# Kernel tuning notes

Measured on AMD Instinct MI355X. Metric: run time of the kernel, lower is better.

Reference implementation:

```python
import math
import jax, jax.numpy as jnp
import numpy as np

D_MODEL = 1024
N_HEADS = 16
D_K = D_MODEL // N_HEADS
LQ, LK, B = 2048, 2048, 2


def setup_inputs() -> dict:
    key = jax.random.key(0)
    ks = jax.random.split(key, 12)
    q = jax.random.normal(ks[0], (LQ, B, D_MODEL), dtype=jnp.float32)
    k = jax.random.normal(ks[1], (LK, B, D_MODEL), dtype=jnp.float32)
    v = jax.random.normal(ks[2], (LK, B, D_MODEL), dtype=jnp.float32)
    # causal mask: scores with mask==0 are filled with -1e9
    mask = jnp.tril(jnp.ones((LQ, LK), dtype=jnp.int32))
    s = 0.02
    w_q = jax.random.normal(ks[3], (D_MODEL, D_MODEL), jnp.float32) * s
    b_q = jnp.zeros((D_MODEL,), jnp.float32)
    w_k = jax.random.normal(ks[4], (D_MODEL, D_MODEL), jnp.float32) * s
    b_k = jnp.zeros((D_MODEL,), jnp.float32)
    w_v = jax.random.normal(ks[5], (D_MODEL, D_MODEL), jnp.float32) * s
    b_v = jnp.zeros((D_MODEL,), jnp.float32)
    w_o = jax.random.normal(ks[6], (D_MODEL, D_MODEL), jnp.float32) * s
    b_o = jnp.zeros((D_MODEL,), jnp.float32)
    return {"query": q, "key": k, "value": v, "mask": mask,
            "w_q": w_q, "b_q": b_q, "w_k": w_k, "b_k": b_k,
            "w_v": w_v, "b_v": b_v, "w_o": w_o, "b_o": b_o}


def reference(query, key, value, mask, w_q, b_q, w_k, b_k, w_v, b_v, w_o, b_o):
    # dropout layers are identity (eval mode)
    Lq, Bsz, D = query.shape
    Lk = key.shape[0]
    scale = math.sqrt(D_K)
    # seq-first linear projections, then [L,B,D] -> [B,H,L,dk]
    def proj(x, w, b, L):
        y = x @ w.T + b
        return y.reshape(L, Bsz, N_HEADS, D_K).transpose(1, 2, 0, 3)
    Q = proj(query, w_q, b_q, Lq)   # [B,H,Lq,dk]
    K = proj(key, w_k, b_k, Lk)     # [B,H,Lk,dk]
    V = proj(value, w_v, b_v, Lk)   # [B,H,Lk,dk]
    scores = jnp.einsum('bhqd,bhkd->bhqk', Q, K) / scale
    m = mask[None, None, :, :]  # 2D mask broadcast path of original
    scores = jnp.where(m == 0, jnp.float32(-1e9), scores)
    attn = jax.nn.softmax(scores, axis=-1)  # [B,H,Lq,Lk]
    out = jnp.einsum('bhqk,bhkd->bhqd', attn, V)  # [B,H,Lq,dk]
    # replicate torch: transpose(0,1) -> [H,B,Lq,dk], flat view to [Lq,B,D]
    out = jnp.transpose(out, (1, 0, 2, 3)).reshape(Lq, Bsz, D)
    output = out @ w_o.T + b_o
    return output, attn
```

## Files before the change

kernel.cpp:

```cpp
#include <hip/hip_runtime.h>
#include <cstdint>

#define DM    1024
#define NH    16
#define DKH   64
#define SEQ   2048
#define BSZ   2
#define MROWS 4096
#define QB    128

typedef __attribute__((ext_vector_type(8))) short bf16x8;
typedef __attribute__((ext_vector_type(4))) float f32x4;

__device__ __forceinline__ f32x4 mfma16(bf16x8 a, bf16x8 b, f32x4 c){
  return __builtin_amdgcn_mfma_f32_16x16x32_bf16(a, b, c, 0, 0, 0);
}

__device__ __forceinline__ ushort f2bf(float f){
  unsigned u = __float_as_uint(f);
  return (ushort)((u + 0x7FFFu + ((u >> 16) & 1u)) >> 16);
}

__device__ __forceinline__ void gload16(const ushort* g, ushort* l){
  __builtin_amdgcn_global_load_lds(
      (const __attribute__((address_space(1))) void*)g,
      (__attribute__((address_space(3))) void*)l, 16, 0, 0);
}

__global__ void cast_all(const float* __restrict__ q, const float* __restrict__ k,
                         const float* __restrict__ v, const float* __restrict__ wq,
                         const float* __restrict__ wk, const float* __restrict__ wv,
                         const float* __restrict__ wo,
                         ushort* __restrict__ qb, ushort* __restrict__ kb,
                         ushort* __restrict__ vb, ushort* __restrict__ wqb,
                         ushort* __restrict__ wkb, ushort* __restrict__ wvb,
                         ushort* __restrict__ wob)
{
  const int NB = (MROWS*DM)/4;
  const int NW = (DM*DM)/4;
  int stride = gridDim.x*blockDim.x;
  for (int i = blockIdx.x*blockDim.x + threadIdx.x; i < 3*NB; i += stride){
    int sel = i >> 20, j = i & (NB-1);
    const float4 x = ((const float4*)(sel==0?q:sel==1?k:v))[j];
    ushort4 o; o.x=f2bf(x.x); o.y=f2bf(x.y); o.z=f2bf(x.z); o.w=f2bf(x.w);
    ((ushort4*)(sel==0?qb:sel==1?kb:vb))[j] = o;
  }
  for (int i = blockIdx.x*blockDim.x + threadIdx.x; i < 4*NW; i += stride){
    int sel = i >> 18, j = i & (NW-1);
    const float4 x = ((const float4*)(sel==0?wq:sel==1?wk:sel==2?wv:wo))[j];
    ushort4 o; o.x=f2bf(x.x); o.y=f2bf(x.y); o.z=f2bf(x.z); o.w=f2bf(x.w);
    ((ushort4*)(sel==0?wqb:sel==1?wkb:sel==2?wvb:wob))[j] = o;
  }
}

template<int OUT_F32>
__device__ __forceinline__ void gemm_body(const ushort* __restrict__ A,
                                          const ushort* __restrict__ W,
                                          const float* __restrict__ bias,
                                          void* __restrict__ outp)
{
  __shared__ ushort As[128*32];
  __shared__ ushort Bs[128*32];
  const int tid = threadIdx.x, w = tid>>6, l = tid&63;
  const int wr = w>>1, wc = w&1, lr = l&15, lg = l>>4;
  const int bm = blockIdx.x, bn = blockIdx.y;
  const ushort* Ab = A + (size_t)bm*128*DM;
  const ushort* Wb = W + (size_t)bn*128*DM;
  f32x4 z4 = {0.f,0.f,0.f,0.f};
  f32x4 acc[4][4];
  #pragma unroll
  for (int i=0;i<4;i++){ acc[i][0]=z4; acc[i][1]=z4; acc[i][2]=z4; acc[i][3]=z4; }

  for (int k0 = 0; k0 < DM; k0 += 32){
    __syncthreads();
    #pragma unroll
    for (int i=0;i<2;i++){
      int idx = w*2+i;
      int row = idx*16 + (l>>2);
      int cg  = (l&3)*8;
      gload16(&Ab[(size_t)row*DM + k0 + cg], &As[idx*512]);
      gload16(&Wb[(size_t)row*DM + k0 + cg], &Bs[idx*512]);
    }
    __syncthreads();
    bf16x8 af[4], bw[4];
    #pragma unroll
    for (int t=0;t<4;t++) af[t] = *(const bf16x8*)&As[(wr*64 + t*16 + lr)*32 + lg*8];
    #pragma unroll
    for (int t=0;t<4;t++) bw[t] = *(const bf16x8*)&Bs[(wc*64 + t*16 + lr)*32 + lg*8];
    #pragma unroll
    for (int tm=0;tm<4;tm++)
      #pragma unroll
      for (int tn=0;tn<4;tn++)
        acc[tm][tn] = mfma16(af[tm], bw[tn], acc[tm][tn]);
  }
  #pragma unroll
  for (int tn=0;tn<4;tn++){
    int col = bn*128 + wc*64 + tn*16 + lr;
    float bv = bias[col];
    #pragma unroll
    for (int tm=0;tm<4;tm++){
      #pragma unroll
      for (int r=0;r<4;r++){
        int row = bm*128 + wr*64 + tm*16 + lg*4 + r;
        float val = acc[tm][tn][r] + bv;
        if (OUT_F32) ((float*)outp)[(size_t)row*DM + col] = val;
        else ((ushort*)outp)[(size_t)row*DM + col] = f2bf(val);
      }
    }
  }
}

__global__ __launch_bounds__(256) void gemm_qkv(
    const ushort* __restrict__ A0, const ushort* __restrict__ A1, const ushort* __restrict__ A2,
    const ushort* __restrict__ W0, const ushort* __restrict__ W1, const ushort* __restrict__ W2,
    const float* __restrict__ b0, const float* __restrict__ b1, const float* __restrict__ b2,
    ushort* __restrict__ O0, ushort* __restrict__ O1, ushort* __restrict__ O2)
{
  int z = blockIdx.z;
  const ushort* A = (z==0)?A0:((z==1)?A1:A2);
  const ushort* W = (z==0)?W0:((z==1)?W1:W2);
  const float*  b = (z==0)?b0:((z==1)?b1:b2);
  ushort*       O = (z==0)?O0:((z==1)?O1:O2);
  gemm_body<0>(A, W, b, O);
}

__global__ __launch_bounds__(256) void gemm_fin(const ushort* __restrict__ A,
                                                const ushort* __restrict__ W,
                                                const float* __restrict__ b,
                                                float* __restrict__ O)
{
  gemm_body<1>(A, W, b, O);
}

__global__ __launch_bounds__(256) void transpose_v(const ushort* __restrict__ Vp,
                                                   ushort* __restrict__ Vt)
{
  __shared__ ushort Ts[64*72];
  const int lt = blockIdx.x;
  const int h  = blockIdx.y;
  const int b  = blockIdx.z;
  const int tid = threadIdx.x;
  const int sr = tid>>3, sc = (tid&7)*8;
  uint4 v0 = *(const uint4*)&Vp[((size_t)(lt*64+sr)*BSZ + b)*DM + h*DKH + sc];
  uint4 v1 = *(const uint4*)&Vp[((size_t)(lt*64+sr+32)*BSZ + b)*DM + h*DKH + sc];
  const ushort* p0 = (const ushort*)&v0;
  const ushort* p1 = (const ushort*)&v1;
  #pragma unroll
  for (int j=0;j<8;j++){
    Ts[(sc+j)*72 + sr]    = p0[j];
    Ts[(sc+j)*72 + sr+32] = p1[j];
  }
  __syncthreads();
  const size_t ob = (size_t)((b*NH+h)*DKH);
  *(uint4*)&Vt[(ob + sr)*SEQ + lt*64 + sc]    = *(const uint4*)&Ts[sr*72 + sc];
  *(uint4*)&Vt[(ob + sr+32)*SEQ + lt*64 + sc] = *(const uint4*)&Ts[(sr+32)*72 + sc];
}

__global__ __launch_bounds__(512) void attn_fused(const ushort* __restrict__ Qp,
                                                  const ushort* __restrict__ Kp,
                                                  const ushort* __restrict__ Vt,
                                                  float* __restrict__ attn,
                                                  ushort* __restrict__ ctx)
{
  __shared__ ushort Ks[64*72];
  __shared__ ushort Vs[64*72];
  __shared__ ushort Ps[8][16*72];
  const int bid0 = blockIdx.x;
  const int bid  = (bid0 & 7)*64 + (bid0 >> 3);
  const int qb = 15 - (bid & 15);
  const int h  = (bid>>4)&15, b = bid>>8;
  const int tid = threadIdx.x, w = tid>>6, l = tid&63;
  const int lr = l&15, lg = l>>4;
  const int q0 = qb*QB;
  const int sr = tid>>3, sc = (tid&7)*8;
  const int ntiles = 2*qb + 2;
  ushort* Pw = &Ps[w][0];
  const size_t attnBase = (size_t)(b*NH+h)*SEQ*SEQ;
  const size_t vtBase   = (size_t)((b*NH+h)*DKH);
  const int qrow = q0 + w*16;
  const int wmax = qrow + 15;

  bf16x8 aq0 = *(const bf16x8*)&Qp[((size_t)(qrow+lr)*BSZ + b)*DM + h*DKH + lg*8];
  bf16x8 aq1 = *(const bf16x8*)&Qp[((size_t)(qrow+lr)*BSZ + b)*DM + h*DKH + 32 + lg*8];

  float rs[4] = {0.f,0.f,0.f,0.f};
  for (int kt = 0; kt < ntiles; kt++){
    __syncthreads();
    *(uint4*)&Ks[sr*72+sc] = *(const uint4*)&Kp[((size_t)(kt*64+sr)*BSZ + b)*DM + h*DKH + sc];
    __syncthreads();
    if (kt*64 <= wmax){
      #pragma unroll
      for (int nt=0; nt<4; nt++){
        f32x4 s4 = {0.f,0.f,0.f,0.f};
        bf16x8 bk0 = *(const bf16x8*)&Ks[(nt*16+lr)*72 + lg*8];
        bf16x8 bk1 = *(const bf16x8*)&Ks[(nt*16+lr)*72 + 32 + lg*8];
        s4 = mfma16(aq0, bk0, s4);
        s4 = mfma16(aq1, bk1, s4);
        int kc = kt*64 + nt*16 + lr;
        #pragma unroll
        for (int r=0;r<4;r++){
          int qr = qrow + lg*4 + r;
          float e = exp2f(s4[r]*0.18033688011112042f);
          rs[r] += (kc <= qr) ? e : 0.f;
        }
      }
    }
  }
  float rinv[4];
  #pragma unroll
  for (int r=0;r<4;r++){
    float vs = rs[r];
    vs += __shfl_xor(vs, 1, 16);
    vs += __shfl_xor(vs, 2, 16);
    vs += __shfl_xor(vs, 4, 16);
    vs += __shfl_xor(vs, 8, 16);
    rinv[r] = 1.0f / vs;
  }

  f32x4 z4 = {0.f,0.f,0.f,0.f};
  f32x4 oacc[4] = {z4,z4,z4,z4};
  for (int kt = 0; kt < ntiles; kt++){
    __syncthreads();
    *(uint4*)&Ks[sr*72+sc] = *(const uint4*)&Kp[((size_t)(kt*64+sr)*BSZ + b)*DM + h*DKH + sc];
    *(uint4*)&Vs[sr*72+sc] = *(const uint4*)&Vt[(vtBase + sr)*SEQ + kt*64 + sc];
    __syncthreads();
    if (kt*64 <= wmax){
      #pragma unroll
      for (int nt=0; nt<4; nt++){
        f32x4 s4 = {0.f,0.f,0.f,0.f};
        bf16x8 bk0 = *(const bf16x8*)&Ks[(nt*16+lr)*72 + lg*8];
        bf16x8 bk1 = *(const bf16x8*)&Ks[(nt*16+lr)*72 + 32 + lg*8];
        s4 = mfma16(aq0, bk0, s4);
        s4 = mfma16(aq1, bk1, s4);
        int kc = kt*64 + nt*16 + lr;
        #pragma unroll
        for (int r=0;r<4;r++){
          int qg = qrow + lg*4 + r;
          float p = (kc <= qg) ? exp2f(s4[r]*0.18033688011112042f)*rinv[r] : 0.f;
          Pw[(lg*4+r)*72 + nt*16 + lr] = f2bf(p);
        }
      }
      #pragma unroll
      for (int pass=0; pass<4; pass++){
        int row = pass*4 + lg;
        ushort4 pv = *(const ushort4*)&Pw[row*72 + lr*4];
        float4 o;
        o.x = __uint_as_float(((unsigned)pv.x) << 16);
        o.y = __uint_as_float(((unsigned)pv.y) << 16);
        o.z = __uint_as_float(((unsigned)pv.z) << 16);
        o.w = __uint_as_float(((unsigned)pv.w) << 16);
        *(float4*)&attn[attnBase + (size_t)(qrow + row)*SEQ + kt*64 + lr*4] = o;
      }
      #pragma unroll
      for (int nt=0; nt<4; nt++){
        #pragma unroll
        for (int ss=0; ss<2; ss++){
          bf16x8 pa = *(const bf16x8*)&Pw[lr*72 + ss*32 + lg*8];
          bf16x8 vb = *(const bf16x8*)&Vs[(nt*16+lr)*72 + ss*32 + lg*8];
          oacc[nt] = mfma16(pa, vb, oacc[nt]);
        }
      }
    } else {
      float4 zz = {0.f,0.f,0.f,0.f};
      #pragma unroll
      for (int pass=0; pass<4; pass++){
        int row = pass*4 + lg;
        *(float4*)&attn[attnBase + (size_t)(qrow + row)*SEQ + kt*64 + lr*4] = zz;
      }
    }
  }
  #pragma unroll
  for (int nt=0;nt<4;nt++){
    #pragma unroll
    for (int r=0;r<4;r++){
      int qg = qrow + lg*4 + r;
      ctx[((size_t)(h*BSZ+b)*SEQ + qg)*DKH + nt*16 + lr] = f2bf(oacc[nt][r]);
    }
  }
  int z0 = ntiles*64;
  if (z0 < SEQ){
    float4 zz = {0.f,0.f,0.f,0.f};
    for (int r16=0; r16<16; r16++){
      float* rowp = attn + attnBase + (size_t)(qrow + r16)*SEQ;
      for (int c = z0 + l*4; c < SEQ; c += 256)
        *(float4*)&rowp[c] = zz;
    }
  }
}

extern "C" void kernel_launch(void* const* d_in, const int* in_sizes, int n_in,
                              void* d_out, int out_size, void* d_ws, size_t ws_size,
                              hipStream_t stream)
{
  (void)in_sizes; (void)n_in; (void)out_size; (void)ws_size;
  const float* q  = (const float*)d_in[0];
  const float* k  = (const float*)d_in[1];
  const float* v  = (const float*)d_in[2];
  const float* wq = (const float*)d_in[4];
  const float* bq = (const float*)d_in[5];
  const float* wk = (const float*)d_in[6];
  const float* bk = (const float*)d_in[7];
  const float* wv = (const float*)d_in[8];
  const float* bv = (const float*)d_in[9];
  const float* wo = (const float*)d_in[10];
  const float* bo = (const float*)d_in[11];

  char* ws = (char*)d_ws;
  const size_t SZ_BIG = (size_t)MROWS*DM*2;
  const size_t SZ_W   = (size_t)DM*DM*2;
  ushort* Qb  = (ushort*)(ws);
  ushort* Kb  = (ushort*)(ws + SZ_BIG);
  ushort* Vb  = (ushort*)(ws + 2*SZ_BIG);
  ushort* Wqb = (ushort*)(ws + 3*SZ_BIG);
  ushort* Wkb = (ushort*)(ws + 3*SZ_BIG + SZ_W);
  ushort* Wvb = (ushort*)(ws + 3*SZ_BIG + 2*SZ_W);
  ushort* Wob = (ushort*)(ws + 3*SZ_BIG + 3*SZ_W);
  ushort* Qp  = (ushort*)(ws + 3*SZ_BIG + 4*SZ_W);
  ushort* Kp  = (ushort*)(ws + 4*SZ_BIG + 4*SZ_W);
  ushort* Vp  = (ushort*)(ws + 5*SZ_BIG + 4*SZ_W);
  ushort* Ctx = (ushort*)(ws + 6*SZ_BIG + 4*SZ_W);
  ushort* Vt  = Qb;

  float* out  = (float*)d_out;
  float* attn = out + (size_t)SEQ*BSZ*DM;

  cast_all<<<2048, 256, 0, stream>>>(q,k,v,wq,wk,wv,wo, Qb,Kb,Vb,Wqb,Wkb,Wvb,Wob);
  dim3 gq(32, 8, 3);
  gemm_qkv<<<gq, 256, 0, stream>>>(Qb,Kb,Vb, Wqb,Wkb,Wvb, bq,bk,bv, Qp,Kp,Vp);
  dim3 gt(32, NH, BSZ);
  transpose_v<<<gt, 256, 0, stream>>>(Vp, Vt);
  attn_fused<<<512, 512, 0, stream>>>(Qp, Kp, Vt, attn, Ctx);
  dim3 gf(32, 8, 1);
  gemm_fin<<<gf, 256, 0, stream>>>(Ctx, Wob, bo, out);
}
```

Measured before the change: 261.1 us.

## Double K/V tile to 128 keys with register prefetch and nontemporal attn stores

Each loop round of the attention kernel now stages 128 keys instead of 64, which halves the number of barrier pairs. The next round's K and V tiles are prefetched into registers while the current round computes. The large attn probability writes switch to nontemporal stores to reduce cache pollution. Block-to-work mapping is changed so the query blocks of one (batch, head) land on the same XCD, and launch bounds now request 4 blocks per CU. The larger LDS footprint and extra prefetch registers may limit occupancy.

```diff
diff --git a/kernel.cpp b/kernel.cpp
--- a/kernel.cpp
+++ b/kernel.cpp
@@ -8,6 +8,7 @@
 #define BSZ   2
 #define MROWS 4096
 #define QB    128
+#define K2    128
 
 typedef __attribute__((ext_vector_type(8))) short bf16x8;
 typedef __attribute__((ext_vector_type(4))) float f32x4;
@@ -25,6 +26,10 @@
   __builtin_amdgcn_global_load_lds(
       (const __attribute__((address_space(1))) void*)g,
       (__attribute__((address_space(3))) void*)l, 16, 0, 0);
+}
+
+__device__ __forceinline__ void ntstore4(float* p, f32x4 v){
+  __builtin_nontemporal_store(v, (f32x4*)p);
 }
 
 __global__ void cast_all(const float* __restrict__ q, const float* __restrict__ k,
@@ -156,134 +161,165 @@
   *(uint4*)&Vt[(ob + sr+32)*SEQ + lt*64 + sc] = *(const uint4*)&Ts[(sr+32)*72 + sc];
 }
 
-__global__ __launch_bounds__(512) void attn_fused(const ushort* __restrict__ Qp,
-                                                  const ushort* __restrict__ Kp,
-                                                  const ushort* __restrict__ Vt,
-                                                  float* __restrict__ attn,
-                                                  ushort* __restrict__ ctx)
-{
-  __shared__ ushort Ks[64*72];
-  __shared__ ushort Vs[64*72];
+__global__ __launch_bounds__(512, 4) void attn_fused(const ushort* __restrict__ Qp,
+                                                     const ushort* __restrict__ Kp,
+                                                     const ushort* __restrict__ Vt,
+                                                     float* __restrict__ attn,
+                                                     ushort* __restrict__ ctx)
+{
+  __shared__ ushort Ks[K2*72];
+  __shared__ ushort Vs[64*136];
   __shared__ ushort Ps[8][16*72];
   const int bid0 = blockIdx.x;
-  const int bid  = (bid0 & 7)*64 + (bid0 >> 3);
-  const int qb = 15 - (bid & 15);
-  const int h  = (bid>>4)&15, b = bid>>8;
+  const int xcd = bid0 & 7, slot = bid0 >> 3;
+  const int grp = xcd + 8*(slot>>4);
+  const int qb  = 15 - (slot & 15);
+  const int h = grp & 15, b = grp >> 4;
   const int tid = threadIdx.x, w = tid>>6, l = tid&63;
   const int lr = l&15, lg = l>>4;
   const int q0 = qb*QB;
-  const int sr = tid>>3, sc = (tid&7)*8;
-  const int ntiles = 2*qb + 2;
+  const int rounds = qb + 1;
   ushort* Pw = &Ps[w][0];
   const size_t attnBase = (size_t)(b*NH+h)*SEQ*SEQ;
   const size_t vtBase   = (size_t)((b*NH+h)*DKH);
   const int qrow = q0 + w*16;
   const int wmax = qrow + 15;
 
+  const int sKr = tid>>3,  sKc = (tid&7)*8;
+  const int sVr = tid>>4,  sVc = (tid&15)*8;
+  const ushort* Kg = Kp + (size_t)b*DM + h*DKH;
+  const ushort* Vg = Vt + vtBase*SEQ;
+
   bf16x8 aq0 = *(const bf16x8*)&Qp[((size_t)(qrow+lr)*BSZ + b)*DM + h*DKH + lg*8];
   bf16x8 aq1 = *(const bf16x8*)&Qp[((size_t)(qrow+lr)*BSZ + b)*DM + h*DKH + 32 + lg*8];
 
   float rs[4] = {0.f,0.f,0.f,0.f};
-  for (int kt = 0; kt < ntiles; kt++){
-    __syncthreads();
-    *(uint4*)&Ks[sr*72+sc] = *(const uint4*)&Kp[((size_t)(kt*64+sr)*BSZ + b)*DM + h*DKH + sc];
-    __syncthreads();
-    if (kt*64 <= wmax){
+  uint4 ka0 = *(const uint4*)&Kg[(size_t)(sKr)*BSZ*DM + sKc];
+  uint4 ka1 = *(const uint4*)&Kg[(size_t)(sKr+64)*BSZ*DM + sKc];
+  for (int r = 0; r < rounds; r++){
+    __syncthreads();
+    *(uint4*)&Ks[sKr*72+sKc]      = ka0;
+    *(uint4*)&Ks[(sKr+64)*72+sKc] = ka1;
+    if (r+1 < rounds){
+      ka0 = *(const uint4*)&Kg[(size_t)((r+1)*K2+sKr)*BSZ*DM + sKc];
+      ka1 = *(const uint4*)&Kg[(size_t)((r+1)*K2+sKr+64)*BSZ*DM + sKc];
+    }
+    __syncthreads();
+    #pragma unroll
+    for (int hh=0; hh<2; hh++){
+      int kbase = r*K2 + hh*64;
+      if (kbase > wmax) break;
       #pragma unroll
       for (int nt=0; nt<4; nt++){
         f32x4 s4 = {0.f,0.f,0.f,0.f};
-        bf16x8 bk0 = *(const bf16x8*)&Ks[(nt*16+lr)*72 + lg*8];
-        bf16x8 bk1 = *(const bf16x8*)&Ks[(nt*16+lr)*72 + 32 + lg*8];
+        bf16x8 bk0 = *(const bf16x8*)&Ks[(hh*64+nt*16+lr)*72 + lg*8];
+        bf16x8 bk1 = *(const bf16x8*)&Ks[(hh*64+nt*16+lr)*72 + 32 + lg*8];
         s4 = mfma16(aq0, bk0, s4);
         s4 = mfma16(aq1, bk1, s4);
-        int kc = kt*64 + nt*16 + lr;
-        #pragma unroll
-        for (int r=0;r<4;r++){
-          int qr = qrow + lg*4 + r;
-          float e = exp2f(s4[r]*0.18033688011112042f);
-          rs[r] += (kc <= qr) ? e : 0.f;
+        int kc = kbase + nt*16 + lr;
+        #pragma unroll
+        for (int r4=0;r4<4;r4++){
+          int qr = qrow + lg*4 + r4;
+          float e = exp2f(s4[r4]*0.18033688011112042f);
+          rs[r4] += (kc <= qr) ? e : 0.f;
         }
       }
     }
   }
   float rinv[4];
   #pragma unroll
-  for (int r=0;r<4;r++){
-    float vs = rs[r];
+  for (int r4=0;r4<4;r4++){
+    float vs = rs[r4];
     vs += __shfl_xor(vs, 1, 16);
     vs += __shfl_xor(vs, 2, 16);
     vs += __shfl_xor(vs, 4, 16);
     vs += __shfl_xor(vs, 8, 16);
-    rinv[r] = 1.0f / vs;
+    rinv[r4] = 1.0f / vs;
   }
 
   f32x4 z4 = {0.f,0.f,0.f,0.f};
   f32x4 oacc[4] = {z4,z4,z4,z4};
-  for (int kt = 0; kt < ntiles; kt++){
-    __syncthreads();
-    *(uint4*)&Ks[sr*72+sc] = *(const uint4*)&Kp[((size_t)(kt*64+sr)*BSZ + b)*DM + h*DKH + sc];
-    *(uint4*)&Vs[sr*72+sc] = *(const uint4*)&Vt[(vtBase + sr)*SEQ + kt*64 + sc];
-    __syncthreads();
-    if (kt*64 <= wmax){
-      #pragma unroll
-      for (int nt=0; nt<4; nt++){
-        f32x4 s4 = {0.f,0.f,0.f,0.f};
-        bf16x8 bk0 = *(const bf16x8*)&Ks[(nt*16+lr)*72 + lg*8];
-        bf16x8 bk1 = *(const bf16x8*)&Ks[(nt*16+lr)*72 + 32 + lg*8];
-        s4 = mfma16(aq0, bk0, s4);
-        s4 = mfma16(aq1, bk1, s4);
-        int kc = kt*64 + nt*16 + lr;
-        #pragma unroll
-        for (int r=0;r<4;r++){
-          int qg = qrow + lg*4 + r;
-          float p = (kc <= qg) ? exp2f(s4[r]*0.18033688011112042f)*rinv[r] : 0.f;
-          Pw[(lg*4+r)*72 + nt*16 + lr] = f2bf(p);
+  uint4 kb0 = *(const uint4*)&Kg[(size_t)(sKr)*BSZ*DM + sKc];
+  uint4 kb1 = *(const uint4*)&Kg[(size_t)(sKr+64)*BSZ*DM + sKc];
+  uint4 vb0 = *(const uint4*)&Vg[(size_t)(sVr)*SEQ + sVc];
+  uint4 vb1 = *(const uint4*)&Vg[(size_t)(sVr+32)*SEQ + sVc];
+  for (int r = 0; r < rounds; r++){
+    __syncthreads();
+    *(uint4*)&Ks[sKr*72+sKc]        = kb0;
+    *(uint4*)&Ks[(sKr+64)*72+sKc]   = kb1;
+    *(uint4*)&Vs[sVr*136+sVc]       = vb0;
+    *(uint4*)&Vs[(sVr+32)*136+sVc]  = vb1;
+    if (r+1 < rounds){
+      kb0 = *(const uint4*)&Kg[(size_t)((r+1)*K2+sKr)*BSZ*DM + sKc];
+      kb1 = *(const uint4*)&Kg[(size_t)((r+1)*K2+sKr+64)*BSZ*DM + sKc];
+      vb0 = *(const uint4*)&Vg[(size_t)(sVr)*SEQ + (r+1)*K2 + sVc];
+      vb1 = *(const uint4*)&Vg[(size_t)(sVr+32)*SEQ + (r+1)*K2 + sVc];
+    }
+    __syncthreads();
+    #pragma unroll
+    for (int hh=0; hh<2; hh++){
+      int kbase = r*K2 + hh*64;
+      if (kbase <= wmax){
+        #pragma unroll
+        for (int nt=0; nt<4; nt++){
+          f32x4 s4 = {0.f,0.f,0.f,0.f};
+          bf16x8 bk0 = *(const bf16x8*)&Ks[(hh*64+nt*16+lr)*72 + lg*8];
+          bf16x8 bk1 = *(const bf16x8*)&Ks[(hh*64+nt*16+lr)*72 + 32 + lg*8];
+          s4 = mfma16(aq0, bk0, s4);
+          s4 = mfma16(aq1, bk1, s4);
+          int kc = kbase + nt*16 + lr;
+          #pragma unroll
+          for (int r4=0;r4<4;r4++){
+            int qg = qrow + lg*4 + r4;
+            float p = (kc <= qg) ? exp2f(s4[r4]*0.18033688011112042f)*rinv[r4] : 0.f;
+            Pw[(lg*4+r4)*72 + nt*16 + lr] = f2bf(p);
+          }
+        }
+        #pragma unroll
+        for (int pass=0; pass<4; pass++){
+          int row = pass*4 + lg;
+          ushort4 pv = *(const ushort4*)&Pw[row*72 + lr*4];
+          f32x4 o;
+          o.x = __uint_as_float(((unsigned)pv.x) << 16);
+          o.y = __uint_as_float(((unsigned)pv.y) << 16);
+          o.z = __uint_as_float(((unsigned)pv.z) << 16);
+          o.w = __uint_as_float(((unsigned)pv.w) << 16);
+          ntstore4(&attn[attnBase + (size_t)(qrow + row)*SEQ + kbase + lr*4], o);
+        }
+        bf16x8 pa0 = *(const bf16x8*)&Pw[lr*72 + lg*8];
+        bf16x8 pa1 = *(const bf16x8*)&Pw[lr*72 + 32 + lg*8];
+        #pragma unroll
+        for (int nt=0; nt<4; nt++){
+          bf16x8 vv0 = *(const bf16x8*)&Vs[(nt*16+lr)*136 + hh*64 + lg*8];
+          bf16x8 vv1 = *(const bf16x8*)&Vs[(nt*16+lr)*136 + hh*64 + 32 + lg*8];
+          oacc[nt] = mfma16(pa0, vv0, oacc[nt]);
+          oacc[nt] = mfma16(pa1, vv1, oacc[nt]);
+        }
+      } else {
+        f32x4 zz = {0.f,0.f,0.f,0.f};
+        #pragma unroll
+        for (int pass=0; pass<4; pass++){
+          int row = pass*4 + lg;
+          ntstore4(&attn[attnBase + (size_t)(qrow + row)*SEQ + kbase + lr*4], zz);
         }
       }
-      #pragma unroll
-      for (int pass=0; pass<4; pass++){
-        int row = pass*4 + lg;
-        ushort4 pv = *(const ushort4*)&Pw[row*72 + lr*4];
-        float4 o;
-        o.x = __uint_as_float(((unsigned)pv.x) << 16);
-        o.y = __uint_as_float(((unsigned)pv.y) << 16);
-        o.z = __uint_as_float(((unsigned)pv.z) << 16);
-        o.w = __uint_as_float(((unsigned)pv.w) << 16);
-        *(float4*)&attn[attnBase + (size_t)(qrow + row)*SEQ + kt*64 + lr*4] = o;
-      }
-      #pragma unroll
-      for (int nt=0; nt<4; nt++){
-        #pragma unroll
-        for (int ss=0; ss<2; ss++){
-          bf16x8 pa = *(const bf16x8*)&Pw[lr*72 + ss*32 + lg*8];
-          bf16x8 vb = *(const bf16x8*)&Vs[(nt*16+lr)*72 + ss*32 + lg*8];
-          oacc[nt] = mfma16(pa, vb, oacc[nt]);
-        }
-      }
-    } else {
-      float4 zz = {0.f,0.f,0.f,0.f};
-      #pragma unroll
-      for (int pass=0; pass<4; pass++){
-        int row = pass*4 + lg;
-        *(float4*)&attn[attnBase + (size_t)(qrow + row)*SEQ + kt*64 + lr*4] = zz;
-      }
     }
   }
   #pragma unroll
   for (int nt=0;nt<4;nt++){
     #pragma unroll
-    for (int r=0;r<4;r++){
-      int qg = qrow + lg*4 + r;
-      ctx[((size_t)(h*BSZ+b)*SEQ + qg)*DKH + nt*16 + lr] = f2bf(oacc[nt][r]);
-    }
-  }
-  int z0 = ntiles*64;
+    for (int r4=0;r4<4;r4++){
+      int qg = qrow + lg*4 + r4;
+      ctx[((size_t)(h*BSZ+b)*SEQ + qg)*DKH + nt*16 + lr] = f2bf(oacc[nt][r4]);
+    }
+  }
+  int z0 = rounds*K2;
   if (z0 < SEQ){
-    float4 zz = {0.f,0.f,0.f,0.f};
+    f32x4 zz = {0.f,0.f,0.f,0.f};
     for (int r16=0; r16<16; r16++){
       float* rowp = attn + attnBase + (size_t)(qrow + r16)*SEQ;
       for (int c = z0 + l*4; c < SEQ; c += 256)
-        *(float4*)&rowp[c] = zz;
+        ntstore4(&rowp[c], zz);
     }
   }
 }
```

Measured after the change: 239.0 us. 1.09x faster.

## Replace two-pass attention with single-pass block storing unnormalized scores in LDS

Applied to the files above, without the earlier changes.

The attention kernel is restructured so each block handles 16 query rows, and its 8 warps split the key tiles among themselves. Each warp computes exp scores once, keeps them as bf16 in a large LDS buffer, and accumulates P·V directly from global K/V without staging. After a cross-warp reduction of the row sums, the attention matrix is normalized and written with nontemporal stores, and the context accumulators are reduced across warps. This removes the second QK^T pass and the per-tile syncthreads, but uses about 66KB of LDS per block, reads K/V from global memory without LDS reuse, and launches 4096 blocks.

```diff
diff --git a/kernel.cpp b/kernel.cpp
--- a/kernel.cpp
+++ b/kernel.cpp
@@ -7,7 +7,8 @@
 #define SEQ   2048
 #define BSZ   2
 #define MROWS 4096
-#define QB    128
+#define SROWS 16
+#define SST   2056
 
 typedef __attribute__((ext_vector_type(8))) short bf16x8;
 typedef __attribute__((ext_vector_type(4))) float f32x4;
@@ -25,6 +26,10 @@
   __builtin_amdgcn_global_load_lds(
       (const __attribute__((address_space(1))) void*)g,
       (__attribute__((address_space(3))) void*)l, 16, 0, 0);
+}
+
+__device__ __forceinline__ void ntstore4(float* p, f32x4 v){
+  __builtin_nontemporal_store(v, (f32x4*)p);
 }
 
 __global__ void cast_all(const float* __restrict__ q, const float* __restrict__ k,
@@ -156,134 +161,121 @@
   *(uint4*)&Vt[(ob + sr+32)*SEQ + lt*64 + sc] = *(const uint4*)&Ts[(sr+32)*72 + sc];
 }
 
-__global__ __launch_bounds__(512) void attn_fused(const ushort* __restrict__ Qp,
-                                                  const ushort* __restrict__ Kp,
-                                                  const ushort* __restrict__ Vt,
-                                                  float* __restrict__ attn,
-                                                  ushort* __restrict__ ctx)
-{
-  __shared__ ushort Ks[64*72];
-  __shared__ ushort Vs[64*72];
-  __shared__ ushort Ps[8][16*72];
+__global__ __launch_bounds__(512, 4) void attn_single(const ushort* __restrict__ Qp,
+                                                      const ushort* __restrict__ Kp,
+                                                      const ushort* __restrict__ Vt,
+                                                      float* __restrict__ attn,
+                                                      ushort* __restrict__ ctx)
+{
+  __shared__ ushort Ss[SROWS*SST];
+  __shared__ float red[8][SROWS];
+  __shared__ float invs[SROWS];
   const int bid0 = blockIdx.x;
-  const int bid  = (bid0 & 7)*64 + (bid0 >> 3);
-  const int qb = 15 - (bid & 15);
-  const int h  = (bid>>4)&15, b = bid>>8;
+  const int xcd = bid0 & 7, slot = bid0 >> 3;
+  const int grp = xcd + 8*(slot & 3);
+  const int s2  = slot >> 2;
+  const int qt  = (s2 & 1) ? (s2 >> 1) : (127 - (s2 >> 1));
+  const int h = grp & 15, b = grp >> 4;
+  const int q0 = qt*SROWS;
+  const int ntiles = (q0 + SROWS - 1)/64 + 1;
   const int tid = threadIdx.x, w = tid>>6, l = tid&63;
   const int lr = l&15, lg = l>>4;
-  const int q0 = qb*QB;
-  const int sr = tid>>3, sc = (tid&7)*8;
-  const int ntiles = 2*qb + 2;
-  ushort* Pw = &Ps[w][0];
   const size_t attnBase = (size_t)(b*NH+h)*SEQ*SEQ;
-  const size_t vtBase   = (size_t)((b*NH+h)*DKH);
-  const int qrow = q0 + w*16;
-  const int wmax = qrow + 15;
-
-  bf16x8 aq0 = *(const bf16x8*)&Qp[((size_t)(qrow+lr)*BSZ + b)*DM + h*DKH + lg*8];
-  bf16x8 aq1 = *(const bf16x8*)&Qp[((size_t)(qrow+lr)*BSZ + b)*DM + h*DKH + 32 + lg*8];
+  const ushort* Kg = Kp + (size_t)b*DM + h*DKH;
+  const ushort* Vg = Vt + (size_t)((b*NH+h)*DKH)*SEQ;
+
+  bf16x8 aq0 = *(const bf16x8*)&Qp[((size_t)(q0+lr)*BSZ + b)*DM + h*DKH + lg*8];
+  bf16x8 aq1 = *(const bf16x8*)&Qp[((size_t)(q0+lr)*BSZ + b)*DM + h*DKH + 32 + lg*8];
 
   float rs[4] = {0.f,0.f,0.f,0.f};
-  for (int kt = 0; kt < ntiles; kt++){
-    __syncthreads();
-    *(uint4*)&Ks[sr*72+sc] = *(const uint4*)&Kp[((size_t)(kt*64+sr)*BSZ + b)*DM + h*DKH + sc];
-    __syncthreads();
-    if (kt*64 <= wmax){
+  f32x4 z4 = {0.f,0.f,0.f,0.f};
+  f32x4 oacc[4] = {z4,z4,z4,z4};
+
+  for (int kt = w; kt < ntiles; kt += 8){
+    #pragma unroll
+    for (int nt=0; nt<4; nt++){
+      f32x4 s4 = {0.f,0.f,0.f,0.f};
+      const ushort* kr = &Kg[(size_t)(kt*64 + nt*16 + lr)*BSZ*DM];
+      bf16x8 bk0 = *(const bf16x8*)&kr[lg*8];
+      bf16x8 bk1 = *(const bf16x8*)&kr[32 + lg*8];
+      s4 = mfma16(aq0, bk0, s4);
+      s4 = mfma16(aq1, bk1, s4);
+      int kc = kt*64 + nt*16 + lr;
+      #pragma unroll
+      for (int r4=0;r4<4;r4++){
+        int qg = q0 + lg*4 + r4;
+        float e = (kc <= qg) ? exp2f(s4[r4]*0.18033688011112042f) : 0.f;
+        rs[r4] += e;
+        Ss[(lg*4+r4)*SST + kt*64 + nt*16 + lr] = f2bf(e);
+      }
+    }
+    #pragma unroll
+    for (int ss=0; ss<2; ss++){
+      bf16x8 pa = *(const bf16x8*)&Ss[lr*SST + kt*64 + ss*32 + lg*8];
       #pragma unroll
       for (int nt=0; nt<4; nt++){
-        f32x4 s4 = {0.f,0.f,0.f,0.f};
-        bf16x8 bk0 = *(const bf16x8*)&Ks[(nt*16+lr)*72 + lg*8];
-        bf16x8 bk1 = *(const bf16x8*)&Ks[(nt*16+lr)*72 + 32 + lg*8];
-        s4 = mfma16(aq0, bk0, s4);
-        s4 = mfma16(aq1, bk1, s4);
-        int kc = kt*64 + nt*16 + lr;
-        #pragma unroll
-        for (int r=0;r<4;r++){
-          int qr = qrow + lg*4 + r;
-          float e = exp2f(s4[r]*0.18033688011112042f);
-          rs[r] += (kc <= qr) ? e : 0.f;
-        }
+        bf16x8 vv = *(const bf16x8*)&Vg[(size_t)(nt*16+lr)*SEQ + kt*64 + ss*32 + lg*8];
+        oacc[nt] = mfma16(pa, vv, oacc[nt]);
       }
     }
   }
-  float rinv[4];
-  #pragma unroll
-  for (int r=0;r<4;r++){
-    float vs = rs[r];
+
+  #pragma unroll
+  for (int r4=0;r4<4;r4++){
+    float vs = rs[r4];
     vs += __shfl_xor(vs, 1, 16);
     vs += __shfl_xor(vs, 2, 16);
     vs += __shfl_xor(vs, 4, 16);
     vs += __shfl_xor(vs, 8, 16);
-    rinv[r] = 1.0f / vs;
-  }
-
-  f32x4 z4 = {0.f,0.f,0.f,0.f};
-  f32x4 oacc[4] = {z4,z4,z4,z4};
-  for (int kt = 0; kt < ntiles; kt++){
-    __syncthreads();
-    *(uint4*)&Ks[sr*72+sc] = *(const uint4*)&Kp[((size_t)(kt*64+sr)*BSZ + b)*DM + h*DKH + sc];
-    *(uint4*)&Vs[sr*72+sc] = *(const uint4*)&Vt[(vtBase + sr)*SEQ + kt*64 + sc];
-    __syncthreads();
-    if (kt*64 <= wmax){
-      #pragma unroll
-      for (int nt=0; nt<4; nt++){
-        f32x4 s4 = {0.f,0.f,0.f,0.f};
-        bf16x8 bk0 = *(const bf16x8*)&Ks[(nt*16+lr)*72 + lg*8];
-        bf16x8 bk1 = *(const bf16x8*)&Ks[(nt*16+lr)*72 + 32 + lg*8];
-        s4 = mfma16(aq0, bk0, s4);
-        s4 = mfma16(aq1, bk1, s4);
-        int kc = kt*64 + nt*16 + lr;
-        #pragma unroll
-        for (int r=0;r<4;r++){
-          int qg = qrow + lg*4 + r;
-          float p = (kc <= qg) ? exp2f(s4[r]*0.18033688011112042f)*rinv[r] : 0.f;
-          Pw[(lg*4+r)*72 + nt*16 + lr] = f2bf(p);
-        }
+    if (lr == 0) red[w][lg*4+r4] = vs;
+  }
+  __syncthreads();
+  if (tid < SROWS){
+    float s = 0.f;
+    #pragma unroll
+    for (int w2=0; w2<8; w2++) s += red[w2][tid];
+    invs[tid] = 1.0f / s;
+  }
+  __syncthreads();
+
+  {
+    const int row = tid>>5, c0 = (tid&31)*4;
+    const float ri = invs[row];
+    const int band = ntiles*64;
+    float* rowp = attn + attnBase + (size_t)(q0+row)*SEQ;
+    for (int c = c0; c < SEQ; c += 128){
+      f32x4 o;
+      if (c < band){
+        ushort4 ev = *(const ushort4*)&Ss[row*SST + c];
+        o.x = __uint_as_float(((unsigned)ev.x) << 16) * ri;
+        o.y = __uint_as_float(((unsigned)ev.y) << 16) * ri;
+        o.z = __uint_as_float(((unsigned)ev.z) << 16) * ri;
+        o.w = __uint_as_float(((unsigned)ev.w) << 16) * ri;
+      } else {
+        o.x = 0.f; o.y = 0.f; o.z = 0.f; o.w = 0.f;
       }
-      #pragma unroll
-      for (int pass=0; pass<4; pass++){
-        int row = pass*4 + lg;
-        ushort4 pv = *(const ushort4*)&Pw[row*72 + lr*4];
-        float4 o;
-        o.x = __uint_as_float(((unsigned)pv.x) << 16);
-        o.y = __uint_as_float(((unsigned)pv.y) << 16);
-        o.z = __uint_as_float(((unsigned)pv.z) << 16);
-        o.w = __uint_as_float(((unsigned)pv.w) << 16);
-        *(float4*)&attn[attnBase + (size_t)(qrow + row)*SEQ + kt*64 + lr*4] = o;
-      }
-      #pragma unroll
-      for (int nt=0; nt<4; nt++){
-        #pragma unroll
-        for (int ss=0; ss<2; ss++){
-          bf16x8 pa = *(const bf16x8*)&Pw[lr*72 + ss*32 + lg*8];
-          bf16x8 vb = *(const bf16x8*)&Vs[(nt*16+lr)*72 + ss*32 + lg*8];
-          oacc[nt] = mfma16(pa, vb, oacc[nt]);
-        }
-      }
-    } else {
-      float4 zz = {0.f,0.f,0.f,0.f};
-      #pragma unroll
-      for (int pass=0; pass<4; pass++){
-        int row = pass*4 + lg;
-        *(float4*)&attn[attnBase + (size_t)(qrow + row)*SEQ + kt*64 + lr*4] = zz;
-      }
-    }
-  }
-  #pragma unroll
-  for (int nt=0;nt<4;nt++){
-    #pragma unroll
-    for (int r=0;r<4;r++){
-      int qg = qrow + lg*4 + r;
-      ctx[((size_t)(h*BSZ+b)*SEQ + qg)*DKH + nt*16 + lr] = f2bf(oacc[nt][r]);
-    }
-  }
-  int z0 = ntiles*64;
-  if (z0 < SEQ){
-    float4 zz = {0.f,0.f,0.f,0.f};
-    for (int r16=0; r16<16; r16++){
-      float* rowp = attn + attnBase + (size_t)(qrow + r16)*SEQ;
-      for (int c = z0 + l*4; c < SEQ; c += 256)
-        *(float4*)&rowp[c] = zz;
+      ntstore4(&rowp[c], o);
+    }
+  }
+  __syncthreads();
+
+  float* fred = (float*)Ss;
+  #pragma unroll
+  for (int nt=0; nt<4; nt++)
+    #pragma unroll
+    for (int r4=0; r4<4; r4++)
+      fred[w*1024 + (lg*4+r4)*64 + nt*16 + lr] = oacc[nt][r4];
+  __syncthreads();
+  {
+    int i0 = tid*2;
+    #pragma unroll
+    for (int j=0; j<2; j++){
+      int i = i0 + j;
+      int row = i>>6, d = i&63;
+      float s = 0.f;
+      #pragma unroll
+      for (int w2=0; w2<8; w2++) s += fred[w2*1024 + i];
+      ctx[((size_t)(h*BSZ+b)*SEQ + q0 + row)*DKH + d] = f2bf(s * invs[row]);
     }
   }
 }
@@ -329,7 +321,7 @@
   gemm_qkv<<<gq, 256, 0, stream>>>(Qb,Kb,Vb, Wqb,Wkb,Wvb, bq,bk,bv, Qp,Kp,Vp);
   dim3 gt(32, NH, BSZ);
   transpose_v<<<gt, 256, 0, stream>>>(Vp, Vt);
-  attn_fused<<<512, 512, 0, stream>>>(Qp, Kp, Vt, attn, Ctx);
+  attn_single<<<4096, 512, 0, stream>>>(Qp, Kp, Vt, attn, Ctx);
   dim3 gf(32, 8, 1);
   gemm_fin<<<gf, 256, 0, stream>>>(Ctx, Wob, bo, out);
 }
```

New measurement: 235.4 us. 9.8% less time.
